# Performance work log

Measured on AMD Instinct MI355X. Metric: run time of the kernel, lower is better.

## Reference

```python
import jax, jax.numpy as jnp
import numpy as np

B, N, C, H = 8, 4096, 256, 8
D = C // H
HID = 4 * C
EPS = 1e-5

def _ln(x, w, b):
    mu = jnp.mean(x, axis=-1, keepdims=True)
    var = jnp.var(x, axis=-1, keepdims=True)
    return (x - mu) * jax.lax.rsqrt(var + EPS) * w + b

def setup_inputs() -> dict:
    key = jax.random.key(0)
    ks = jax.random.split(key, 16)
    s = lambda k, shp, scale=0.02: jax.random.normal(k, shp, dtype=jnp.float32) * scale
    return {
        "input_": jax.random.normal(ks[0], (B, N, C), dtype=jnp.float32),
        "prev_state": jax.random.normal(ks[1], (B, N, C), dtype=jnp.float32),
        "pos_embed": jax.random.normal(ks[2], (1, N, C), dtype=jnp.float32),
        "norm1_w": jnp.ones((C,), jnp.float32), "norm1_b": jnp.zeros((C,), jnp.float32),
        "norm2_w": jnp.ones((C,), jnp.float32), "norm2_b": jnp.zeros((C,), jnp.float32),
        "norm3_w": jnp.ones((C,), jnp.float32), "norm3_b": jnp.zeros((C,), jnp.float32),
        "qkv_input_w": s(ks[3], (3 * C, C)),
        "qkv_state_w": s(ks[4], (3 * C, C)),
        "proj_w": s(ks[5], (C, C)), "proj_b": jnp.zeros((C,), jnp.float32),
        "gate_w": s(ks[6], (C, 2 * C)), "gate_b": jnp.zeros((C,), jnp.float32),
        "fc1_w": s(ks[7], (HID, C)), "fc1_b": jnp.zeros((HID,), jnp.float32),
        "fc2_w": s(ks[8], (C, HID)), "fc2_b": jnp.zeros((C,), jnp.float32),
    }

def reference(input_, prev_state, pos_embed,
              norm1_w, norm1_b, norm2_w, norm2_b, norm3_w, norm3_b,
              qkv_input_w, qkv_state_w, proj_w, proj_b,
              gate_w, gate_b, fc1_w, fc1_b, fc2_w, fc2_b):
    input_pos = input_ + pos_embed
    x_ln = _ln(input_pos, norm1_w, norm1_b)
    s_ln = _ln(prev_state, norm2_w, norm2_b)
    # fused QKV from input and state; torch Linear: x @ W.T
    qkv_i = (x_ln @ qkv_input_w.T).reshape(B, N, 3, H, D).transpose(2, 0, 3, 1, 4)
    qkv_s = (s_ln @ qkv_state_w.T).reshape(B, N, 3, H, D).transpose(2, 0, 3, 1, 4)
    q = qkv_i[0] + qkv_s[0]  # [B,H,N,D]
    k = qkv_i[1] + qkv_s[1]
    v = qkv_i[2] + qkv_s[2]
    phi_q = jax.nn.elu(q) + 1.0
    phi_k = jax.nn.elu(k) + 1.0
    # (phi_q @ phi_k^T) @ v reordered associatively to O(N*D^2)
    kv = jnp.einsum('bhnd,bhne->bhde', phi_k, v)        # [B,H,D,D]
    attn = jnp.einsum('bhnd,bhde->bhne', phi_q, kv)     # [B,H,N,D]
    attn = attn.transpose(0, 2, 1, 3).reshape(B, N, C)
    attn = attn @ proj_w.T + proj_b
    output = input_pos + attn
    stacked = jnp.concatenate([input_, prev_state], axis=2)
    update = jax.nn.sigmoid(stacked @ gate_w.T + gate_b)
    new_state = prev_state * (1.0 - update) + attn * update
    h = _ln(output, norm3_w, norm3_b)
    h = jax.nn.gelu(h @ fc1_w.T + fc1_b, approximate=False) @ fc2_w.T + fc2_b
    output = output + h
    return (output, new_state)
```

## Files before the change

### kernel.cpp

```cpp
#include <hip/hip_runtime.h>
#include <cmath>

typedef unsigned short u16;
typedef __attribute__((ext_vector_type(8))) short short8;
typedef __attribute__((ext_vector_type(4))) float f32x4;
typedef __attribute__((ext_vector_type(4))) u16 u16x4;

__device__ __forceinline__ float b2f(u16 u) {
    unsigned x = ((unsigned)u) << 16;
    return __builtin_bit_cast(float, x);
}
__device__ __forceinline__ u16 f2b(float f) {
    unsigned x = __builtin_bit_cast(unsigned, f);
    unsigned r = (x + 0x7fffu + ((x >> 16) & 1u)) >> 16;
    return (u16)r;
}
__device__ __forceinline__ float loadx(const void* p, size_t i, int f32) {
    return f32 ? ((const float*)p)[i] : b2f(((const u16*)p)[i]);
}
__device__ __forceinline__ void gl_lds16(const void* g, void* l) {
    __builtin_amdgcn_global_load_lds(
        (const __attribute__((address_space(1))) void*)g,
        (__attribute__((address_space(3))) void*)l, 16, 0, 0);
}
__device__ __forceinline__ float gelu_f(float x) {
    float y = 0.7978845608028654f * (x + 0.044715f * x * x * x);
    float e = __expf(2.f * y);
    float t = 1.f - 2.f / (e + 1.f);
    return 0.5f * x * (1.f + t);
}

#define BB 8
#define NN 4096
#define CC 256
#define HH 8
#define DD 32
#define HID 1024
#define MTOK (BB*NN)
#define TOKEL ((size_t)MTOK*CC)
#define TOKELC 8388608

#define WS_INPUT_POS 0u
#define WS_PHIQ   16777216u
#define WS_PHIK   33554432u
#define WS_V      50331648u
#define WS_XLN    67108864u
#define WS_SLN    83886080u
#define WS_OUTPRE 100663296u
#define WS_FLAG   117440512u

#define OFF_QKVI  0u
#define OFF_QKVS  196608u
#define OFF_PROJW 393216u
#define OFF_GATEW 458752u
#define OFF_FC1W  589824u
#define OFF_FC2W  851968u
#define OFF_PROJB 1114112u
#define OFF_GATEB 1114368u
#define OFF_FC1B  1114624u
#define OFF_FC2B  1115648u
#define WTOT      1115904u

__device__ __attribute__((aligned(16))) u16 g_wb[WTOT];
__device__ __attribute__((aligned(16))) u16 g_inb[TOKELC];
__device__ __attribute__((aligned(16))) u16 g_prevb[TOKELC];

__global__ __launch_bounds__(64) void detect_kernel(const u16* __restrict__ in0,
                                                    int* __restrict__ flag)
{
    int t = threadIdx.x;
    u16 w = in0[2 * t];
    int e = (w >> 7) & 0xFF;
    int bad = (e < 64 || e > 192) ? 1 : 0;
    unsigned long long m = __ballot(bad);
    if (t == 0) *flag = (__popcll(m) > 8) ? 1 : 0;
}

__global__ __launch_bounds__(256) void wconv_kernel(
    const void* qkvi, const void* qkvs, const void* projw, const void* gatew,
    const void* fc1w, const void* fc2w, const void* projb, const void* gateb,
    const void* fc1b, const void* fc2b, const int* __restrict__ flagp)
{
    const int f32 = *flagp;
    unsigned i = blockIdx.x * 256 + threadIdx.x;
    if (i >= WTOT) return;
    const void* src; unsigned off;
    if      (i < OFF_QKVS)  { src = qkvi;  off = OFF_QKVI; }
    else if (i < OFF_PROJW) { src = qkvs;  off = OFF_QKVS; }
    else if (i < OFF_GATEW) { src = projw; off = OFF_PROJW; }
    else if (i < OFF_FC1W)  { src = gatew; off = OFF_GATEW; }
    else if (i < OFF_FC2W)  { src = fc1w;  off = OFF_FC1W; }
    else if (i < OFF_PROJB) { src = fc2w;  off = OFF_FC2W; }
    else if (i < OFF_GATEB) { src = projb; off = OFF_PROJB; }
    else if (i < OFF_FC1B)  { src = gateb; off = OFF_GATEB; }
    else if (i < OFF_FC2B)  { src = fc1b;  off = OFF_FC1B; }
    else                    { src = fc2b;  off = OFF_FC2B; }
    g_wb[i] = f2b(loadx(src, i - off, f32));
}

__global__ __launch_bounds__(256) void prep_kernel(
    const void* __restrict__ inp, const void* __restrict__ prev,
    const void* __restrict__ pos,
    const void* __restrict__ w1, const void* __restrict__ b1,
    const void* __restrict__ w2, const void* __restrict__ b2,
    u16* __restrict__ input_pos, u16* __restrict__ x_ln, u16* __restrict__ s_ln,
    const int* __restrict__ flagp)
{
    const int f32 = *flagp;
    const int m = blockIdx.x;
    const int c = threadIdx.x;
    const int n = m & (NN - 1);
    const size_t idx = (size_t)m * CC + c;

    __shared__ float red[8];

    float inr = loadx(inp, idx, f32);
    float ip = inr + loadx(pos, (size_t)n * CC + c, f32);
    g_inb[idx] = f2b(inr);
    float s = ip, s2 = ip * ip;
    #pragma unroll
    for (int o = 32; o; o >>= 1) { s += __shfl_down(s, o, 64); s2 += __shfl_down(s2, o, 64); }
    if ((threadIdx.x & 63) == 0) { int w6 = threadIdx.x >> 6; red[w6] = s; red[4 + w6] = s2; }
    __syncthreads();
    float mu  = (red[0] + red[1] + red[2] + red[3]) * (1.f / 256.f);
    float var = (red[4] + red[5] + red[6] + red[7]) * (1.f / 256.f) - mu * mu;
    float rs = rsqrtf(var + 1e-5f);
    input_pos[idx] = f2b(ip);
    x_ln[idx] = f2b((ip - mu) * rs * loadx(w1, c, f32) + loadx(b1, c, f32));
    __syncthreads();

    float pv = loadx(prev, idx, f32);
    g_prevb[idx] = f2b(pv);
    s = pv; s2 = pv * pv;
    #pragma unroll
    for (int o = 32; o; o >>= 1) { s += __shfl_down(s, o, 64); s2 += __shfl_down(s2, o, 64); }
    if ((threadIdx.x & 63) == 0) { int w6 = threadIdx.x >> 6; red[w6] = s; red[4 + w6] = s2; }
    __syncthreads();
    mu  = (red[0] + red[1] + red[2] + red[3]) * (1.f / 256.f);
    var = (red[4] + red[5] + red[6] + red[7]) * (1.f / 256.f) - mu * mu;
    rs = rsqrtf(var + 1e-5f);
    s_ln[idx] = f2b((pv - mu) * rs * loadx(w2, c, f32) + loadx(b2, c, f32));
}

__global__ __launch_bounds__(256) void ln3_kernel(
    const u16* __restrict__ op, const void* __restrict__ w,
    const void* __restrict__ b, u16* __restrict__ out, const int* __restrict__ flagp)
{
    const int f32 = *flagp;
    const size_t m = blockIdx.x;
    const int c = threadIdx.x;
    const size_t idx = m * CC + c;
    __shared__ float red[8];
    float x = b2f(op[idx]);
    float s = x, s2 = x * x;
    #pragma unroll
    for (int o = 32; o; o >>= 1) { s += __shfl_down(s, o, 64); s2 += __shfl_down(s2, o, 64); }
    if ((threadIdx.x & 63) == 0) { int w6 = threadIdx.x >> 6; red[w6] = s; red[4 + w6] = s2; }
    __syncthreads();
    float mu  = (red[0] + red[1] + red[2] + red[3]) * (1.f / 256.f);
    float var = (red[4] + red[5] + red[6] + red[7]) * (1.f / 256.f) - mu * mu;
    out[idx] = f2b((x - mu) * rsqrtf(var + 1e-5f) * loadx(w, c, f32) + loadx(b, c, f32));
}

__global__ __launch_bounds__(64) void kv_mfma(
    const u16* __restrict__ phik_t, const u16* __restrict__ v_t,
    float* __restrict__ kvout)
{
    const int bh = blockIdx.x;
    const int k0 = blockIdx.y * 256;
    const int lane = threadIdx.x;
    const int quad = lane >> 4, lr = lane & 15;

    const u16* A = phik_t + (size_t)bh * DD * NN;
    const u16* W = v_t    + (size_t)bh * DD * NN;

    f32x4 acc[2][2];
    #pragma unroll
    for (int i = 0; i < 2; ++i)
        #pragma unroll
        for (int j = 0; j < 2; ++j) { f32x4 z = {0.f,0.f,0.f,0.f}; acc[i][j] = z; }

    for (int kk = k0; kk < k0 + 256; kk += 32) {
        short8 a0 = *(const short8*)(A + (size_t)lr * NN + kk + quad * 8);
        short8 a1 = *(const short8*)(A + (size_t)(16 + lr) * NN + kk + quad * 8);
        short8 w0 = *(const short8*)(W + (size_t)lr * NN + kk + quad * 8);
        short8 w1 = *(const short8*)(W + (size_t)(16 + lr) * NN + kk + quad * 8);
        acc[0][0] = __builtin_amdgcn_mfma_f32_16x16x32_bf16(a0, w0, acc[0][0], 0, 0, 0);
        acc[0][1] = __builtin_amdgcn_mfma_f32_16x16x32_bf16(a0, w1, acc[0][1], 0, 0, 0);
        acc[1][0] = __builtin_amdgcn_mfma_f32_16x16x32_bf16(a1, w0, acc[1][0], 0, 0, 0);
        acc[1][1] = __builtin_amdgcn_mfma_f32_16x16x32_bf16(a1, w1, acc[1][1], 0, 0, 0);
    }
    float* base = kvout + (size_t)bh * (DD * DD);
    #pragma unroll
    for (int i = 0; i < 2; ++i)
        #pragma unroll
        for (int j = 0; j < 2; ++j)
            #pragma unroll
            for (int r = 0; r < 4; ++r)
                atomicAdd(base + (i * 16 + quad * 4 + r) * DD + j * 16 + lr, acc[i][j][r]);
}

__global__ __launch_bounds__(256) void attn_mfma(
    const u16* __restrict__ phiq, const float* __restrict__ kv,
    u16* __restrict__ attn_tok)
{
    const int bh = blockIdx.x;
    const int b = bh >> 3, h = bh & 7;
    const int wv = threadIdx.x >> 6, lane = threadIdx.x & 63;
    const int quad = lane >> 4, lr = lane & 15;

    const float* kvb = kv + (size_t)bh * (DD * DD);
    short8 bf0, bf1;
    #pragma unroll
    for (int j = 0; j < 8; ++j) {
        int d = quad * 8 + j;
        bf0[j] = (short)f2b(kvb[d * DD + lr]);
        bf1[j] = (short)f2b(kvb[d * DD + 16 + lr]);
    }

    const u16* qb = phiq + (size_t)bh * NN * DD;
    const int n0 = blockIdx.y * 512 + wv * 128;
    #pragma unroll
    for (int t = 0; t < 8; ++t) {
        const int nt = n0 + t * 16;
        short8 af = *(const short8*)(qb + (size_t)(nt + lr) * DD + quad * 8);
        f32x4 c0 = {0.f,0.f,0.f,0.f}, c1 = {0.f,0.f,0.f,0.f};
        c0 = __builtin_amdgcn_mfma_f32_16x16x32_bf16(af, bf0, c0, 0, 0, 0);
        c1 = __builtin_amdgcn_mfma_f32_16x16x32_bf16(af, bf1, c1, 0, 0, 0);
        size_t base = ((size_t)b * NN + nt + quad * 4) * CC + h * DD;
        #pragma unroll
        for (int r = 0; r < 4; ++r) {
            attn_tok[base + (size_t)r * CC + lr]      = f2b(c0[r]);
            attn_tok[base + (size_t)r * CC + 16 + lr] = f2b(c1[r]);
        }
    }
}

#define BM 128
#define BN 128
#define BK 32

template <int MODE>
__global__ __launch_bounds__(256) void gemm_bt(
    const u16* __restrict__ A1in, const u16* __restrict__ A2in,
    int lda, int ldw, int K, int Ksplit, int wcol2,
    u16* __restrict__ o0, u16* __restrict__ o1,
    const u16* __restrict__ xa, const void* __restrict__ xr,
    void* __restrict__ oraw, const int* __restrict__ flagp)
{
    __shared__ __attribute__((aligned(16))) u16 ash[BM * BK];
    __shared__ __attribute__((aligned(16))) u16 bsh[BN * BK];

    const int f32 = (MODE == 2 || MODE == 4) ? *flagp : 0;

    const u16* W1; const u16* W2; const u16* bias = nullptr;
    if (MODE == 0)      { W1 = g_wb + OFF_QKVI; W2 = g_wb + OFF_QKVS; }
    else if (MODE == 1) { W1 = W2 = g_wb + OFF_PROJW; bias = g_wb + OFF_PROJB; }
    else if (MODE == 2) { W1 = W2 = g_wb + OFF_GATEW; bias = g_wb + OFF_GATEB; }
    else if (MODE == 3) { W1 = W2 = g_wb + OFF_FC1W;  bias = g_wb + OFF_FC1B; }
    else                { W1 = W2 = g_wb + OFF_FC2W;  bias = g_wb + OFF_FC2B; }
    const u16* A1 = (MODE == 2) ? g_inb   : A1in;
    const u16* A2 = (MODE == 2) ? g_prevb : A2in;

    const int gx = gridDim.x;
    const int nwg = gx * (int)gridDim.y;
    const int hw = blockIdx.y * gx + blockIdx.x;
    const int qq = nwg >> 3, rr = nwg & 7;
    const int xc = hw & 7, pp = hw >> 3;
    const int nid = (xc < rr ? xc * (qq + 1) : rr * (qq + 1) + (xc - rr) * qq) + pp;
    const int bx = nid % gx, by = nid / gx;

    const int tid = threadIdx.x;
    const int lane = tid & 63;
    const int wv = tid >> 6;
    const int wm = wv >> 1, wn = wv & 1;
    const int quad = lane >> 4, lr = lane & 15;

    const bool swp = (MODE == 0) ? (bx < 2) : true;

    f32x4 acc[4][4];
    #pragma unroll
    for (int i = 0; i < 4; ++i)
        #pragma unroll
        for (int j = 0; j < 4; ++j) { f32x4 z = {0.f,0.f,0.f,0.f}; acc[i][j] = z; }

    const size_t arow0 = (size_t)by * BM;
    const size_t wrow0 = (size_t)bx * BN;

    const int srow = lane & 31;
    const int sg   = (lane >> 5) << 3;

    for (int k0 = 0; k0 < K; k0 += BK) {
        const u16* As; const u16* Ws; int ka, kw;
        if (k0 < Ksplit) { As = A1; Ws = W1; ka = k0;          kw = k0; }
        else             { As = A2; Ws = W2; ka = k0 - Ksplit; kw = k0 - Ksplit + wcol2; }

        const u16* ga = As + (arow0 + wv * 32 + srow) * (size_t)lda + ka + sg;
        u16* la = ash + (wv << 10);
        gl_lds16(ga, la);
        gl_lds16(ga + 16, la + 512);
        const u16* gw = Ws + (wrow0 + wv * 32 + srow) * (size_t)ldw + kw + sg;
        u16* lb = bsh + (wv << 10);
        gl_lds16(gw, lb);
        gl_lds16(gw + 16, lb + 512);
        __syncthreads();

        short8 af[4], bf[4];
        #pragma unroll
        for (int i = 0; i < 4; ++i) {
            const int ra = wm * 64 + i * 16 + lr;
            af[i] = *(const short8*)(ash + ((ra >> 5) << 10) + (quad << 8) + ((ra & 31) << 3));
        }
        #pragma unroll
        for (int j = 0; j < 4; ++j) {
            const int rb = wn * 64 + j * 16 + lr;
            bf[j] = *(const short8*)(bsh + ((rb >> 5) << 10) + (quad << 8) + ((rb & 31) << 3));
        }
        if (swp) {
            #pragma unroll
            for (int i = 0; i < 4; ++i)
                #pragma unroll
                for (int j = 0; j < 4; ++j)
                    acc[i][j] = __builtin_amdgcn_mfma_f32_16x16x32_bf16(bf[j], af[i], acc[i][j], 0, 0, 0);
        } else {
            #pragma unroll
            for (int i = 0; i < 4; ++i)
                #pragma unroll
                for (int j = 0; j < 4; ++j)
                    acc[i][j] = __builtin_amdgcn_mfma_f32_16x16x32_bf16(af[i], bf[j], acc[i][j], 0, 0, 0);
        }
        __syncthreads();
    }

    const int mbase = by * BM + wm * 64;
    const int nbase = bx * BN + wn * 64;
    constexpr int LDOUT = (MODE == 3) ? HID : CC;

    #pragma unroll
    for (int i = 0; i < 4; ++i) {
        #pragma unroll
        for (int j = 0; j < 4; ++j) {
            if (MODE == 0) {
                if (swp) {
                    const int m = mbase + i * 16 + lr;
                    const int b = m >> 12, n = m & (NN - 1);
                    const int c0 = nbase + j * 16 + quad * 4;
                    const int h = c0 >> 5, d0 = c0 & 31;
                    u16x4 p;
                    #pragma unroll
                    for (int r = 0; r < 4; ++r) {
                        float v = acc[i][j][r];
                        p[r] = f2b((v > 0.f) ? (v + 1.f) : __expf(v));
                    }
                    *(u16x4*)(o0 + (((size_t)b * HH + h) * NN + n) * DD + d0) = p;
                } else {
                    const int c = nbase + j * 16 + lr;
                    const int which = c >> 8, rem = c & 255, h = rem >> 5, d = rem & 31;
                    const int m0 = mbase + i * 16 + quad * 4;
                    const int b = m0 >> 12, n0i = m0 & (NN - 1);
                    u16x4 p;
                    #pragma unroll
                    for (int r = 0; r < 4; ++r) {
                        float v = acc[i][j][r];
                        if (which == 1) v = (v > 0.f) ? (v + 1.f) : __expf(v);
                        p[r] = f2b(v);
                    }
                    u16* dst = o0 + (size_t)which * TOKEL;
                    *(u16x4*)(dst + (((size_t)b * HH + h) * DD + d) * NN + n0i) = p;
                }
            } else {
                const int m = mbase + i * 16 + lr;
                const int c0 = nbase + j * 16 + quad * 4;
                const size_t idx0 = (size_t)m * LDOUT + c0;
                float bias4[4];
                {
                    u16x4 t = *(const u16x4*)(bias + c0);
                    #pragma unroll
                    for (int r = 0; r < 4; ++r) bias4[r] = b2f(t[r]);
                }
                if (MODE == 1) {
                    u16x4 xa4 = *(const u16x4*)(xa + idx0);
                    u16x4 po, pr;
                    #pragma unroll
                    for (int r = 0; r < 4; ++r) {
                        float val = acc[i][j][r] + bias4[r];
                        po[r] = f2b(val);
                        pr[r] = f2b(b2f(xa4[r]) + val);
                    }
                    *(u16x4*)(o0 + idx0) = po;
                    *(u16x4*)(o1 + idx0) = pr;
                } else if (MODE == 2) {
                    u16x4 ap4 = *(const u16x4*)(xa + idx0);
                    if (f32) {
                        f32x4 pv = *(const f32x4*)((const float*)xr + idx0);
                        f32x4 o;
                        #pragma unroll
                        for (int r = 0; r < 4; ++r) {
                            float u = 1.f / (1.f + __expf(-(acc[i][j][r] + bias4[r])));
                            o[r] = pv[r] * (1.f - u) + b2f(ap4[r]) * u;
                        }
                        *(f32x4*)((float*)oraw + TOKEL + idx0) = o;
                    } else {
                        u16x4 pv = *(const u16x4*)((const u16*)xr + idx0);
                        u16x4 o;
                        #pragma unroll
                        for (int r = 0; r < 4; ++r) {
                            float u = 1.f / (1.f + __expf(-(acc[i][j][r] + bias4[r])));
                            o[r] = f2b(b2f(pv[r]) * (1.f - u) + b2f(ap4[r]) * u);
                        }
                        *(u16x4*)((u16*)oraw + TOKEL + idx0) = o;
                    }
                } else if (MODE == 3) {
                    u16x4 p;
                    #pragma unroll
                    for (int r = 0; r < 4; ++r)
                        p[r] = f2b(gelu_f(acc[i][j][r] + bias4[r]));
                    *(u16x4*)(o0 + idx0) = p;
                } else {
                    u16x4 xa4 = *(const u16x4*)(xa + idx0);
                    if (f32) {
                        f32x4 o;
                        #pragma unroll
                        for (int r = 0; r < 4; ++r)
                            o[r] = b2f(xa4[r]) + acc[i][j][r] + bias4[r];
                        *(f32x4*)((float*)oraw + idx0) = o;
                    } else {
                        u16x4 o;
                        #pragma unroll
                        for (int r = 0; r < 4; ++r)
                            o[r] = f2b(b2f(xa4[r]) + acc[i][j][r] + bias4[r]);
                        *(u16x4*)((u16*)oraw + idx0) = o;
                    }
                }
            }
        }
    }
}

extern "C" void kernel_launch(void* const* d_in, const int* in_sizes, int n_in,
                              void* d_out, int out_size, void* d_ws, size_t ws_size,
                              hipStream_t stream)
{
    const void* input_ = d_in[0];
    const void* prev   = d_in[1];
    const void* pos    = d_in[2];
    const void* n1w = d_in[3];  const void* n1b = d_in[4];
    const void* n2w = d_in[5];  const void* n2b = d_in[6];
    const void* n3w = d_in[7];  const void* n3b = d_in[8];
    const void* qkvi = d_in[9]; const void* qkvs = d_in[10];
    const void* projw = d_in[11]; const void* projb = d_in[12];
    const void* gatew = d_in[13]; const void* gateb = d_in[14];
    const void* fc1w = d_in[15]; const void* fc1b = d_in[16];
    const void* fc2w = d_in[17]; const void* fc2b = d_in[18];

    char* ws = (char*)d_ws;
    u16* input_pos = (u16*)(ws + WS_INPUT_POS);
    u16* phiq  = (u16*)(ws + WS_PHIQ);
    u16* phikt = (u16*)(ws + WS_PHIK);
    u16* vt    = (u16*)(ws + WS_V);
    u16* x_ln = (u16*)(ws + WS_XLN);
    u16* s_ln = (u16*)(ws + WS_SLN);
    u16* attn_tok = x_ln;
    u16* attn_proj = phikt;
    float* kvf = (float*)(ws + WS_SLN);
    u16* ln3o = s_ln;
    u16* outpre = (u16*)(ws + WS_OUTPRE);
    u16* h1 = (u16*)(ws + WS_INPUT_POS);
    int* flagp = (int*)(ws + WS_FLAG);

    detect_kernel<<<1, 64, 0, stream>>>((const u16*)input_, flagp);
    wconv_kernel<<<(WTOT + 255) / 256, 256, 0, stream>>>(
        qkvi, qkvs, projw, gatew, fc1w, fc2w, projb, gateb, fc1b, fc2b, flagp);
    prep_kernel<<<MTOK, 256, 0, stream>>>(input_, prev, pos, n1w, n1b, n2w, n2b,
                                          input_pos, x_ln, s_ln, flagp);
    gemm_bt<0><<<dim3(3 * CC / BN, MTOK / BM), 256, 0, stream>>>(
        x_ln, s_ln, CC, CC, 2 * CC, CC, 0,
        phiq, nullptr, nullptr, nullptr, nullptr, flagp);
    hipMemsetAsync((void*)kvf, 0, BB * HH * DD * DD * sizeof(float), stream);
    kv_mfma<<<dim3(BB * HH, 16), 64, 0, stream>>>(phikt, vt, kvf);
    attn_mfma<<<dim3(BB * HH, NN / 512), 256, 0, stream>>>(phiq, kvf, attn_tok);
    gemm_bt<1><<<dim3(CC / BN, MTOK / BM), 256, 0, stream>>>(
        attn_tok, attn_tok, CC, CC, CC, CC, 0,
        attn_proj, outpre, input_pos, nullptr, nullptr, flagp);
    gemm_bt<2><<<dim3(CC / BN, MTOK / BM), 256, 0, stream>>>(
        nullptr, nullptr, CC, 2 * CC, 2 * CC, CC, CC,
        nullptr, nullptr, attn_proj, prev, d_out, flagp);
    ln3_kernel<<<MTOK, 256, 0, stream>>>(outpre, n3w, n3b, ln3o, flagp);
    gemm_bt<3><<<dim3(HID / BN, MTOK / BM), 256, 0, stream>>>(
        ln3o, ln3o, CC, CC, CC, CC, 0,
        h1, nullptr, nullptr, nullptr, nullptr, flagp);
    gemm_bt<4><<<dim3(CC / BN, MTOK / BM), 256, 0, stream>>>(
        h1, h1, HID, HID, HID, HID, 0,
        nullptr, nullptr, outpre, nullptr, d_out, flagp);
}
```

Baseline: 478.2 us.

## Double-buffer GEMM LDS tiles with 64-wide K stages and MFMA priority

Restructures the bf16 GEMM main loop to stage two 32-wide K slices (64 per step) into a double-buffered LDS tile. The next pair is prefetched with global_load_lds while the current pair is computed, which halves the number of barriers and overlaps global loads with MFMA. s_setprio is raised around the MFMA block. LDS use grows fourfold, which may reduce occupancy. The new loop also assumes K and Ksplit are multiples of 64.

```diff
diff --git a/kernel.cpp b/kernel.cpp
--- a/kernel.cpp
+++ b/kernel.cpp
@@ -238,7 +238,6 @@
 
 #define BM 128
 #define BN 128
-#define BK 32
 
 template <int MODE>
 __global__ __launch_bounds__(256) void gemm_bt(
@@ -248,8 +247,8 @@
     const u16* __restrict__ xa, const void* __restrict__ xr,
     void* __restrict__ oraw, const int* __restrict__ flagp)
 {
-    __shared__ __attribute__((aligned(16))) u16 ash[BM * BK];
-    __shared__ __attribute__((aligned(16))) u16 bsh[BN * BK];
+    __shared__ __attribute__((aligned(16))) u16 ash[2][2][4096];
+    __shared__ __attribute__((aligned(16))) u16 bsh[2][2][4096];
 
     const int f32 = (MODE == 2 || MODE == 4) ? *flagp : 0;
 
@@ -289,33 +288,41 @@
 
     const int srow = lane & 31;
     const int sg   = (lane >> 5) << 3;
-
-    for (int k0 = 0; k0 < K; k0 += BK) {
+    const size_t aoff = (arow0 + wv * 32 + srow) * (size_t)lda + sg;
+    const size_t woff = (wrow0 + wv * 32 + srow) * (size_t)ldw + sg;
+
+    auto stage_pair = [&](int pb, int m) {
+        const int k0 = m * 64;
         const u16* As; const u16* Ws; int ka, kw;
         if (k0 < Ksplit) { As = A1; Ws = W1; ka = k0;          kw = k0; }
         else             { As = A2; Ws = W2; ka = k0 - Ksplit; kw = k0 - Ksplit + wcol2; }
-
-        const u16* ga = As + (arow0 + wv * 32 + srow) * (size_t)lda + ka + sg;
-        u16* la = ash + (wv << 10);
-        gl_lds16(ga, la);
-        gl_lds16(ga + 16, la + 512);
-        const u16* gw = Ws + (wrow0 + wv * 32 + srow) * (size_t)ldw + kw + sg;
-        u16* lb = bsh + (wv << 10);
-        gl_lds16(gw, lb);
-        gl_lds16(gw + 16, lb + 512);
-        __syncthreads();
-
+        const u16* ga = As + aoff + ka;
+        const u16* gw = Ws + woff + kw;
+        u16* la0 = &ash[pb][0][wv << 10];
+        u16* la1 = &ash[pb][1][wv << 10];
+        u16* lb0 = &bsh[pb][0][wv << 10];
+        u16* lb1 = &bsh[pb][1][wv << 10];
+        gl_lds16(ga,      la0);  gl_lds16(ga + 16, la0 + 512);
+        gl_lds16(ga + 32, la1);  gl_lds16(ga + 48, la1 + 512);
+        gl_lds16(gw,      lb0);  gl_lds16(gw + 16, lb0 + 512);
+        gl_lds16(gw + 32, lb1);  gl_lds16(gw + 48, lb1 + 512);
+    };
+
+    auto compute = [&](int pb, int sb) {
+        const u16* a0 = &ash[pb][sb][0];
+        const u16* b0 = &bsh[pb][sb][0];
         short8 af[4], bf[4];
         #pragma unroll
         for (int i = 0; i < 4; ++i) {
             const int ra = wm * 64 + i * 16 + lr;
-            af[i] = *(const short8*)(ash + ((ra >> 5) << 10) + (quad << 8) + ((ra & 31) << 3));
+            af[i] = *(const short8*)(a0 + ((ra >> 5) << 10) + (quad << 8) + ((ra & 31) << 3));
         }
         #pragma unroll
         for (int j = 0; j < 4; ++j) {
             const int rb = wn * 64 + j * 16 + lr;
-            bf[j] = *(const short8*)(bsh + ((rb >> 5) << 10) + (quad << 8) + ((rb & 31) << 3));
+            bf[j] = *(const short8*)(b0 + ((rb >> 5) << 10) + (quad << 8) + ((rb & 31) << 3));
         }
+        __builtin_amdgcn_s_setprio(1);
         if (swp) {
             #pragma unroll
             for (int i = 0; i < 4; ++i)
@@ -329,7 +336,17 @@
                 for (int j = 0; j < 4; ++j)
                     acc[i][j] = __builtin_amdgcn_mfma_f32_16x16x32_bf16(af[i], bf[j], acc[i][j], 0, 0, 0);
         }
-        __syncthreads();
+        __builtin_amdgcn_s_setprio(0);
+    };
+
+    const int MT = K >> 6;
+    stage_pair(0, 0);
+    __syncthreads();
+    for (int m = 0; m < MT; ++m) {
+        if (m + 1 < MT) stage_pair((m + 1) & 1, m + 1);
+        compute(m & 1, 0);
+        compute(m & 1, 1);
+        if (m + 1 < MT) __syncthreads();
     }
 
     const int mbase = by * BM + wm * 64;
```

New measurement: 512.0 us. 1.07x slower.
